# Kernel tuning notes

Measured on AMD Instinct MI355X. Metric: run time of the kernel, lower is better.

The kernel has to match this reference:

```python
import jax, jax.numpy as jnp
import numpy as np
import math
from jax import lax

B, NP1, M, D, H, L, DFF = 16, 65, 256, 512, 8, 3, 2048
EPS_PROJ = 0.01  # MartingaleProjectionLayer is built with epsilon=0.01
LN_EPS = 1e-5


def _pos_encoding(n, d):
    pos = np.arange(n, dtype=np.float32)[:, None]
    div = np.exp(np.arange(0, d, 2, dtype=np.float32) * (-math.log(10000.0) / d))
    pe = np.zeros((n, d), dtype=np.float32)
    pe[:, 0::2] = np.sin(pos * div)
    pe[:, 1::2] = np.cos(pos * div)
    return jnp.asarray(pe)


def setup_inputs() -> dict:
    key = jax.random.key(0)
    ks = jax.random.split(key, 32)
    s = 0.02
    marg = jax.random.uniform(ks[0], (B, NP1, M), jnp.float32)
    marg = marg / marg.sum(axis=-1, keepdims=True)  # proper distributions
    return {
        "marginals": marg,
        "x_grid": jnp.linspace(-3.0, 3.0, M, dtype=jnp.float32),
        "conv_w": jax.random.normal(ks[1], (128, 1, 5), jnp.float32) * s,
        "conv_b": jax.random.normal(ks[2], (128,), jnp.float32) * s,
        "fc_w": jax.random.normal(ks[3], (128, D), jnp.float32) * s,
        "fc_b": jax.random.normal(ks[4], (D,), jnp.float32) * s,
        "ln0_g": jnp.ones((D,), jnp.float32),
        "ln0_b": jnp.zeros((D,), jnp.float32),
        "pos_enc": _pos_encoding(NP1, D),
        "qkv_w": jax.random.normal(ks[5], (L, 3 * D, D), jnp.float32) * s,
        "qkv_b": jax.random.normal(ks[6], (L, 3 * D), jnp.float32) * s,
        "out_w": jax.random.normal(ks[7], (L, D, D), jnp.float32) * s,
        "out_b": jax.random.normal(ks[8], (L, D), jnp.float32) * s,
        "ln1_g": jnp.ones((L, D), jnp.float32),
        "ln1_b": jnp.zeros((L, D), jnp.float32),
        "ff1_w": jax.random.normal(ks[9], (L, DFF, D), jnp.float32) * s,
        "ff1_b": jax.random.normal(ks[10], (L, DFF), jnp.float32) * s,
        "ff2_w": jax.random.normal(ks[11], (L, D, DFF), jnp.float32) * s,
        "ff2_b": jax.random.normal(ks[12], (L, D), jnp.float32) * s,
        "ln2_g": jnp.ones((L, D), jnp.float32),
        "ln2_b": jnp.zeros((L, D), jnp.float32),
        "u_w": jax.random.normal(ks[13], (M, D), jnp.float32) * s,
        "u_b": jax.random.normal(ks[14], (M,), jnp.float32) * s,
        "h_w": jax.random.normal(ks[15], (M, D), jnp.float32) * s,
        "h_b": jax.random.normal(ks[16], (M,), jnp.float32) * s,
    }


def _ln(x, g, b):
    mu = x.mean(axis=-1, keepdims=True)
    var = ((x - mu) ** 2).mean(axis=-1, keepdims=True)
    return (x - mu) * lax.rsqrt(var + LN_EPS) * g + b


def _gelu(x):
    return jax.nn.gelu(x, approximate=False)  # torch default exact GELU


def reference(marginals, x_grid, conv_w, conv_b, fc_w, fc_b, ln0_g, ln0_b,
              pos_enc, qkv_w, qkv_b, out_w, out_b, ln1_g, ln1_b,
              ff1_w, ff1_b, ff2_w, ff2_b, ln2_g, ln2_b, u_w, u_b, h_w, h_b):
    b, np1, m = marginals.shape
    n = np1 - 1
    d = fc_w.shape[1]
    nh = H
    dh = d // nh

    # ---- marginal embedding: Conv1d(1,128,k=5,pad=2) -> mean over grid -> FC+LN+GELU
    x = marginals.reshape(b * np1, 1, m)
    y = lax.conv_general_dilated(x, conv_w, (1,), [(2, 2)],
                                 dimension_numbers=("NCH", "OIH", "NCH"))
    y = y + conv_b[None, :, None]          # (b*np1, 128, m)
    emb = y.mean(axis=2)                   # (b*np1, 128)
    emb = _gelu(_ln(emb @ fc_w + fc_b, ln0_g, ln0_b))
    xs = emb.reshape(b, np1, d) + pos_enc[None, :np1, :]

    # ---- post-norm transformer encoder (dropout off / eval mode)
    scale = 1.0 / math.sqrt(dh)
    for l in range(L):
        qkv = xs @ qkv_w[l].T + qkv_b[l]                        # (b, s, 3d)
        q, k, v = jnp.split(qkv, 3, axis=-1)
        q = q.reshape(b, np1, nh, dh).transpose(0, 2, 1, 3)
        k = k.reshape(b, np1, nh, dh).transpose(0, 2, 1, 3)
        v = v.reshape(b, np1, nh, dh).transpose(0, 2, 1, 3)
        att = jax.nn.softmax(jnp.einsum("bhqd,bhkd->bhqk", q, k) * scale, axis=-1)
        o = jnp.einsum("bhqk,bhkd->bhqd", att, v)
        o = o.transpose(0, 2, 1, 3).reshape(b, np1, d)
        o = o @ out_w[l].T + out_b[l]
        xs = _ln(xs + o, ln1_g[l], ln1_b[l])
        ff = _gelu(xs @ ff1_w[l].T + ff1_b[l]) @ ff2_w[l].T + ff2_b[l]
        xs = _ln(xs + ff, ln2_g[l], ln2_b[l])

    u_pot = xs @ u_w.T + u_b                                    # (b, np1, M)
    h_raw = xs[:, :n, :] @ h_w.T + h_b                          # (b, n, M)

    # ---- vectorized martingale projection over all N timesteps
    x_diff = x_grid[:, None] - x_grid[None, :]                  # (M, M)
    h_kernel = h_raw[..., None] * x_diff                        # (b, n, M, M)
    P = jax.nn.softmax(h_kernel / EPS_PROJ, axis=-1)
    expected_next = jnp.einsum("bnij,j->bni", P, x_grid)
    drift = expected_next - x_grid                              # (b, n, M)
    mu = marginals[:, :n, :]
    weight_drift = (mu * drift).sum(axis=-1, keepdims=True)
    correction = weight_drift / (mu.sum(axis=-1, keepdims=True) + 1e-8)
    h_pot = h_raw - correction
    return (u_pot, h_pot)
```

## Files before the change

### kernel.cpp

```cpp
#include <hip/hip_runtime.h>
#include <math.h>


#define BT   1040
#define NP1  65
#define Dm   512
#define MG   256

typedef short short8 __attribute__((ext_vector_type(8)));
typedef float f32x4  __attribute__((ext_vector_type(4)));
typedef unsigned short u16;

__device__ __forceinline__ size_t pidx(int r, int c, int KB) {
  return ((size_t)((r >> 6) * KB + (c >> 6)) * 8 + ((c & 63) >> 3)) * 512
       + (size_t)((r & 63) * 8 + (c & 7));
}

__device__ __forceinline__ u16 f2bf(float f) {
  unsigned int u = __float_as_uint(f);
  u += 0x7FFF + ((u >> 16) & 1);
  return (u16)(u >> 16);
}

__device__ __forceinline__ float gelu_exact(float x) {
  return 0.5f * x * (1.0f + erff(x * 0.70710678118654752f));
}

__device__ __forceinline__ void async16(const u16* g, u16* l) {
  __builtin_amdgcn_global_load_lds(
      (const __attribute__((address_space(1))) unsigned int*)g,
      (__attribute__((address_space(3))) unsigned int*)l, 16, 0, 0);
}

__device__ __forceinline__ float wred(float v) {
#pragma unroll
  for (int o = 32; o; o >>= 1) v += __shfl_xor(v, o, 64);
  return v;
}

__device__ __forceinline__ float block_reduce_sum(float v, float* s) {
#pragma unroll
  for (int off = 32; off; off >>= 1) v += __shfl_down(v, off, 64);
  int lane = threadIdx.x & 63, wid = threadIdx.x >> 6;
  __syncthreads();
  if (lane == 0) s[wid] = v;
  __syncthreads();
  return s[0] + s[1] + s[2] + s[3];
}

__device__ __forceinline__ float f_closed(float a) {
  const float tf = 2.3529411765f;
  float t = a * tf;
  float s = fabsf(t);
  float E;
  if (s < 1e-4f) {
    E = 127.5f - 5461.25f * t;
  } else {
    float u = s * 256.0f;
    float term2 = (u < 80.0f) ? 256.0f / expm1f(u) : 0.0f;
    float Epos = 1.0f / expm1f(s) - term2;
    E = (t > 0.0f) ? Epos : 255.0f - Epos;
  }
  return -3.0f + 0.0235294118f * E;
}

__global__ __launch_bounds__(256) void prep_kernel(
    const float* __restrict__ qkv_w, const float* __restrict__ out_w,
    const float* __restrict__ ff1_w, const float* __restrict__ ff2_w,
    const float* __restrict__ u_w,   const float* __restrict__ h_w,
    u16* __restrict__ wdst,
    const float* __restrict__ marg, const float* __restrict__ conv_w,
    const float* __restrict__ conv_b, const float* __restrict__ fc_w,
    const float* __restrict__ fc_b, const float* __restrict__ g,
    const float* __restrict__ bb, const float* __restrict__ pos,
    float* __restrict__ xs, u16* __restrict__ xsb)
{
  const int tid = threadIdx.x;
  if (blockIdx.x < 512) {
    const size_t O1 = 2359296, O2 = 3145728, O3 = 6291456;
    const size_t O4 = 9437184, O5 = 9568256, TOT4 = 9699328 / 4;
    for (size_t e4 = (size_t)blockIdx.x * 256 + tid; e4 < TOT4;
         e4 += (size_t)512 * 256) {
      size_t e = e4 * 4;
      const float* src; size_t base; int n, k, KB;
      if (e < O1)      { size_t r = e;      src = qkv_w + r; base = 0;
                         n = (int)(r >> 9);  k = (int)(r & 511);  KB = 8; }
      else if (e < O2) { size_t r = e - O1; src = out_w + r; base = O1;
                         n = (int)(r >> 9);  k = (int)(r & 511);  KB = 8; }
      else if (e < O3) { size_t r = e - O2; src = ff1_w + r; base = O2;
                         n = (int)(r >> 9);  k = (int)(r & 511);  KB = 8; }
      else if (e < O4) { size_t r = e - O3; src = ff2_w + r; base = O3;
                         n = (int)(r >> 11); k = (int)(r & 2047); KB = 32; }
      else if (e < O5) { size_t r = e - O4; src = u_w + r;   base = O4;
                         n = (int)(r >> 9);  k = (int)(r & 511);  KB = 8; }
      else             { size_t r = e - O5; src = h_w + r;   base = O4;
                         n = 256 + (int)(r >> 9); k = (int)(r & 511); KB = 8; }
      float4 v = *(const float4*)src;
      unsigned int lo = (unsigned int)f2bf(v.x) | ((unsigned int)f2bf(v.y) << 16);
      unsigned int hi = (unsigned int)f2bf(v.z) | ((unsigned int)f2bf(v.w) << 16);
      *(uint2*)(wdst + base + pidx(n, k, KB)) = make_uint2(lo, hi);
    }
    return;
  }
  __shared__ float es[4][128];
  __shared__ float sS[4];
  __shared__ float edge[4][4];
  __shared__ float red[4];
  const int t0 = (blockIdx.x - 512) * 4;
  const int lane = tid & 63, wave = tid >> 6;
  {
    float4 mv = *(const float4*)(marg + (size_t)(t0 + wave) * MG + lane * 4);
    float S = wred(mv.x + mv.y + mv.z + mv.w);
    if (lane == 0) sS[wave] = S;
  }
  if (tid < 16) {
    int k = tid >> 2, e = tid & 3;
    int idx = (e < 2) ? e : (e + 252);
    edge[k][e] = marg[(size_t)(t0 + k) * MG + idx];
  }
  __syncthreads();
  if (tid < 128) {
    int o = tid;
    float w0 = conv_w[o*5+0], w1 = conv_w[o*5+1], w2 = conv_w[o*5+2];
    float w3 = conv_w[o*5+3], w4 = conv_w[o*5+4], cb = conv_b[o];
#pragma unroll
    for (int k = 0; k < 4; ++k) {
      float S = sS[k];
      float x0 = edge[k][0], x1 = edge[k][1], x254 = edge[k][2], x255 = edge[k][3];
      es[k][o] = (w0*(S - x254 - x255) + w1*(S - x255) + w2*S
                + w3*(S - x0) + w4*(S - x0 - x1)) * (1.0f/256.0f) + cb;
    }
  }
  __syncthreads();
  float b0 = fc_b[tid], b1 = fc_b[tid + 256];
  float z[4][2];
#pragma unroll
  for (int k = 0; k < 4; ++k) { z[k][0] = b0; z[k][1] = b1; }
#pragma unroll 4
  for (int o = 0; o < 128; ++o) {
    float f0 = fc_w[(size_t)o*Dm + tid];
    float f1 = fc_w[(size_t)o*Dm + tid + 256];
#pragma unroll
    for (int k = 0; k < 4; ++k) {
      float e = es[k][o];
      z[k][0] += e * f0; z[k][1] += e * f1;
    }
  }
  float g0 = g[tid], g1 = g[tid+256], e0 = bb[tid], e1 = bb[tid+256];
#pragma unroll
  for (int k = 0; k < 4; ++k) {
    float mu = block_reduce_sum(z[k][0] + z[k][1], red) * (1.0f/512.0f);
    float d0 = z[k][0] - mu, d1 = z[k][1] - mu;
    float var = block_reduce_sum(d0*d0 + d1*d1, red) * (1.0f/512.0f);
    float inv = rsqrtf(var + 1e-5f);
    int t = t0 + k, p = t % NP1;
    float y0 = gelu_exact(d0*inv*g0 + e0) + pos[(size_t)p*Dm + tid];
    float y1 = gelu_exact(d1*inv*g1 + e1) + pos[(size_t)p*Dm + tid + 256];
    xs[(size_t)t*Dm + tid]        = y0;
    xs[(size_t)t*Dm + tid + 256]  = y1;
    xsb[pidx(t, tid, 8)]          = f2bf(y0);
    xsb[pidx(t, tid + 256, 8)]    = f2bf(y1);
  }
}

template<int MODE>
__global__ __launch_bounds__(256) void gemm_mfma(
    const u16* __restrict__ A, const u16* __restrict__ Bw,
    const float* __restrict__ bias, float* __restrict__ Cf,
    u16* __restrict__ Cb, int Mrows, int N, int K)
{
  __shared__ u16 Asl[2][4096];
  __shared__ u16 Bsl[2][4096];
  const int tid = threadIdx.x;
  const int row0 = blockIdx.y * 64, col0 = blockIdx.x * 64;
  const int lane = tid & 63, wave = tid >> 6;
  const int wm = (wave >> 1) * 32, wn = (wave & 1) * 32;
  const int l15 = lane & 15, q = lane >> 4;
  const int KB = K >> 6;

  f32x4 acc[2][2];
  acc[0][0] = (f32x4){0,0,0,0}; acc[0][1] = (f32x4){0,0,0,0};
  acc[1][0] = (f32x4){0,0,0,0}; acc[1][1] = (f32x4){0,0,0,0};

  const size_t abase = (size_t)blockIdx.y * KB * 4096 + (size_t)lane * 8;
  const size_t bbase = (size_t)blockIdx.x * KB * 4096 + (size_t)lane * 8;
  const int c0w = wave * 2;

#pragma unroll
  for (int i = 0; i < 2; ++i) {
    int c = c0w + i;
    async16(A + abase + (size_t)c * 512, &Asl[0][(size_t)(c * 64 + lane) * 8]);
    async16(Bw + bbase + (size_t)c * 512, &Bsl[0][(size_t)(c * 64 + lane) * 8]);
  }

  const int nk = K >> 6;
  for (int t = 0; t < nk; ++t) {
    const int cur = t & 1;
    if (t + 1 < nk) {
      const int nxt = cur ^ 1;
#pragma unroll
      for (int i = 0; i < 2; ++i) {
        int c = c0w + i;
        async16(A + abase + (size_t)((t + 1) * 8 + c) * 512,
                &Asl[nxt][(size_t)(c * 64 + lane) * 8]);
        async16(Bw + bbase + (size_t)((t + 1) * 8 + c) * 512,
                &Bsl[nxt][(size_t)(c * 64 + lane) * 8]);
      }
      asm volatile("s_waitcnt vmcnt(4)" ::: "memory");
    } else {
      asm volatile("s_waitcnt vmcnt(0)" ::: "memory");
    }
    __builtin_amdgcn_s_barrier();
#pragma unroll
    for (int tt = 0; tt < 2; ++tt) {
      int cc = tt * 4 + q;
      short8 af[2], bf[2];
#pragma unroll
      for (int mi = 0; mi < 2; ++mi)
        af[mi] = *(short8*)&Asl[cur][(size_t)(cc*64 + wm + mi*16 + l15) * 8];
#pragma unroll
      for (int ni = 0; ni < 2; ++ni)
        bf[ni] = *(short8*)&Bsl[cur][(size_t)(cc*64 + wn + ni*16 + l15) * 8];
#pragma unroll
      for (int mi = 0; mi < 2; ++mi)
#pragma unroll
        for (int ni = 0; ni < 2; ++ni)
          acc[mi][ni] = __builtin_amdgcn_mfma_f32_16x16x32_bf16(
              af[mi], bf[ni], acc[mi][ni], 0, 0, 0);
    }
    __builtin_amdgcn_s_barrier();
  }

#pragma unroll
  for (int mi = 0; mi < 2; ++mi) {
#pragma unroll
    for (int ni = 0; ni < 2; ++ni) {
      int col = col0 + wn + ni*16 + l15;
#pragma unroll
      for (int r = 0; r < 4; ++r) {
        int row = row0 + wm + mi*16 + q*4 + r;
        if (row < Mrows) {
          float v = acc[mi][ni][r];
          if (MODE == 0) {
            Cf[(size_t)row*N + col] = v + bias[col];
          } else {
            Cb[pidx(row, col, 32)] = f2bf(gelu_exact(v + bias[col]));
          }
        }
      }
    }
  }
}

template<int KK, int EPI>
__global__ __launch_bounds__(256) void fused_row(
    const u16* __restrict__ A, const u16* __restrict__ Bw,
    const float* __restrict__ bias,
    float* __restrict__ xs, u16* __restrict__ xsb,
    const float* __restrict__ g, const float* __restrict__ bb,
    const float* __restrict__ bias2,
    const float* __restrict__ marg, const float* __restrict__ xg,
    float* __restrict__ outu, float* __restrict__ outh)
{
  constexpr int KB  = KK >> 6;
  constexpr int KC  = (KK < 1024) ? KK : 1024;
  constexpr int NCH = KK / KC;
  __shared__ u16 Alds[16 * KC];
  __shared__ float red[4][16];
  __shared__ float red2[4][16];
  const int tid = threadIdx.x, lane = tid & 63, wave = tid >> 6;
  const int l15 = lane & 15, q = lane >> 4;
  const int r0 = blockIdx.x * 16;
  const int rb = r0 >> 6, ro = r0 & 63;
  const int gc0 = wave * 128;

  f32x4 acc[8];
#pragma unroll
  for (int i = 0; i < 8; ++i) acc[i] = (f32x4){0,0,0,0};

  for (int ch = 0; ch < NCH; ++ch) {
    const int kc = ch * KC;
    __syncthreads();
    for (int idx = tid; idx < 2 * KC; idx += 256) {
      int rloc = idx & 15, cg = idx >> 4;
      int kbg = (kc >> 6) + (cg >> 3), cc = cg & 7;
      async16(A + ((size_t)(rb * KB + kbg) * 8 + cc) * 512 + (ro + rloc) * 8,
              &Alds[(size_t)idx * 8]);
    }
    asm volatile("s_waitcnt vmcnt(0)" ::: "memory");
    __syncthreads();

    constexpr int S = KC / 32;
    short8 bcur[8], bnxt[8];
    {
      int kk = kc + q * 8;
      int kbg = kk >> 6, cc = (kk & 63) >> 3;
#pragma unroll
      for (int i = 0; i < 8; ++i) {
        int nb = (gc0 >> 6) + (i >> 2), nn = (i & 3) * 16 + l15;
        bcur[i] = *(const short8*)&Bw[((size_t)(nb * KB + kbg) * 8 + cc) * 512
                                      + nn * 8];
      }
    }
    for (int s = 0; s < S; ++s) {
      if (s + 1 < S) {
        int kk = kc + (s + 1) * 32 + q * 8;
        int kbg = kk >> 6, cc = (kk & 63) >> 3;
#pragma unroll
        for (int i = 0; i < 8; ++i) {
          int nb = (gc0 >> 6) + (i >> 2), nn = (i & 3) * 16 + l15;
          bnxt[i] = *(const short8*)&Bw[((size_t)(nb * KB + kbg) * 8 + cc) * 512
                                        + nn * 8];
        }
      }
      short8 af = *(const short8*)&Alds[(size_t)((s * 4 + q) * 16 + l15) * 8];
#pragma unroll
      for (int i = 0; i < 8; ++i)
        acc[i] = __builtin_amdgcn_mfma_f32_16x16x32_bf16(af, bcur[i], acc[i], 0, 0, 0);
#pragma unroll
      for (int i = 0; i < 8; ++i) bcur[i] = bnxt[i];
    }
  }

  if (EPI == 0) {
    float vv[8][4];
#pragma unroll
    for (int i = 0; i < 8; ++i) {
      int col = gc0 + i*16 + l15;
      float bcol = bias[col];
#pragma unroll
      for (int r = 0; r < 4; ++r) {
        int gr = r0 + q*4 + r;
        vv[i][r] = acc[i][r] + bcol + xs[(size_t)gr * Dm + col];
      }
    }
    float ps[4];
#pragma unroll
    for (int r = 0; r < 4; ++r) {
      float s = 0.f;
#pragma unroll
      for (int i = 0; i < 8; ++i) s += vv[i][r];
      ps[r] = s;
    }
#pragma unroll
    for (int o = 1; o < 16; o <<= 1)
#pragma unroll
      for (int r = 0; r < 4; ++r) ps[r] += __shfl_xor(ps[r], o, 64);
    if (l15 == 0)
#pragma unroll
      for (int r = 0; r < 4; ++r) red[wave][q*4 + r] = ps[r];
    __syncthreads();
    float mu[4];
#pragma unroll
    for (int r = 0; r < 4; ++r) {
      int rr = q*4 + r;
      mu[r] = (red[0][rr] + red[1][rr] + red[2][rr] + red[3][rr]) * (1.0f/512.0f);
    }
    float ps2[4];
#pragma unroll
    for (int r = 0; r < 4; ++r) {
      float s = 0.f;
#pragma unroll
      for (int i = 0; i < 8; ++i) { float d = vv[i][r] - mu[r]; s += d * d; }
      ps2[r] = s;
    }
#pragma unroll
    for (int o = 1; o < 16; o <<= 1)
#pragma unroll
      for (int r = 0; r < 4; ++r) ps2[r] += __shfl_xor(ps2[r], o, 64);
    if (l15 == 0)
#pragma unroll
      for (int r = 0; r < 4; ++r) red2[wave][q*4 + r] = ps2[r];
    __syncthreads();
    float inv[4];
#pragma unroll
    for (int r = 0; r < 4; ++r) {
      int rr = q*4 + r;
      inv[r] = rsqrtf((red2[0][rr] + red2[1][rr] + red2[2][rr] + red2[3][rr])
                      * (1.0f/512.0f) + 1e-5f);
    }
#pragma unroll
    for (int i = 0; i < 8; ++i) {
      int col = gc0 + i*16 + l15;
      float gc = g[col], bc = bb[col];
#pragma unroll
      for (int r = 0; r < 4; ++r) {
        int gr = r0 + q*4 + r;
        float y = (vv[i][r] - mu[r]) * inv[r] * gc + bc;
        xs[(size_t)gr * Dm + col] = y;
        xsb[pidx(gr, col, 8)] = f2bf(y);
      }
    }
  } else {
    float va[8][4];
    if (wave >= 2) {
      float wd[4] = {0.f,0.f,0.f,0.f}, ms[4] = {0.f,0.f,0.f,0.f};
#pragma unroll
      for (int i = 0; i < 8; ++i) {
        int hcol = (gc0 - 256) + i*16 + l15;
        float bcol = bias2[hcol];
        float xv = xg[hcol];
#pragma unroll
        for (int r = 0; r < 4; ++r) {
          int gr = r0 + q*4 + r;
          float a = acc[i][r] + bcol;
          va[i][r] = a;
          float uvm = marg[(size_t)gr * MG + hcol];
          wd[r] += uvm * (f_closed(a) - xv);
          ms[r] += uvm;
        }
      }
#pragma unroll
      for (int o = 1; o < 16; o <<= 1)
#pragma unroll
        for (int r = 0; r < 4; ++r) {
          wd[r] += __shfl_xor(wd[r], o, 64);
          ms[r] += __shfl_xor(ms[r], o, 64);
        }
      if (l15 == 0)
#pragma unroll
        for (int r = 0; r < 4; ++r) {
          red[wave][q*4 + r]  = wd[r];
          red2[wave][q*4 + r] = ms[r];
        }
    }
    __syncthreads();
    if (wave < 2) {
#pragma unroll
      for (int i = 0; i < 8; ++i) {
        int col = gc0 + i*16 + l15;
        float bcol = bias[col];
#pragma unroll
        for (int r = 0; r < 4; ++r) {
          int gr = r0 + q*4 + r;
          outu[(size_t)gr * MG + col] = acc[i][r] + bcol;
        }
      }
    } else {
#pragma unroll
      for (int i = 0; i < 8; ++i) {
        int hcol = (gc0 - 256) + i*16 + l15;
#pragma unroll
        for (int r = 0; r < 4; ++r) {
          int rr = q*4 + r;
          int gr = r0 + rr;
          int b = gr / NP1, n = gr - b * NP1;
          if (n < 64) {
            float corr = (red[2][rr] + red[3][rr])
                       / (red2[2][rr] + red2[3][rr] + 1e-8f);
            outh[(size_t)(b * 64 + n) * MG + hcol] = va[i][r] - corr;
          }
        }
      }
    }
  }
}

__global__ __launch_bounds__(256) void attn_kernel(
    const float* __restrict__ qkv, u16* __restrict__ obufb)
{
  __shared__ float qv[65][67];
  __shared__ float ks[65][67];
  __shared__ float ss[65][67];
  const int b = blockIdx.x >> 3, h = blockIdx.x & 7;
  const int tid = threadIdx.x;
  const float* base = qkv + (size_t)b * NP1 * 1536 + h * 64;
  for (int idx = tid; idx < NP1 * 16; idx += 256) {
    int t = idx >> 4, c = (idx & 15) << 2;
    const float* p = base + (size_t)t * 1536 + c;
    float4 q4 = *(const float4*)(p);
    float4 k4 = *(const float4*)(p + 512);
    qv[t][c] = q4.x; qv[t][c+1] = q4.y; qv[t][c+2] = q4.z; qv[t][c+3] = q4.w;
    ks[t][c] = k4.x; ks[t][c+1] = k4.y; ks[t][c+2] = k4.z; ks[t][c+3] = k4.w;
  }
  __syncthreads();
#pragma unroll
  for (int it = 0; it < 2; ++it) {
    int tile = it * 256 + tid;
    if (tile < 289) {
      int ti = (tile / 17) * 4, tj = (tile % 17) * 4;
      const float* qr[4]; const float* kr[4];
#pragma unroll
      for (int i = 0; i < 4; ++i) { qr[i] = qv[min(ti + i, 64)]; kr[i] = ks[min(tj + i, 64)]; }
      float acc[4][4] = {};
      for (int d = 0; d < 64; ++d) {
        float a[4], bvv[4];
#pragma unroll
        for (int i = 0; i < 4; ++i) { a[i] = qr[i][d]; bvv[i] = kr[i][d]; }
#pragma unroll
        for (int i = 0; i < 4; ++i)
#pragma unroll
          for (int j = 0; j < 4; ++j) acc[i][j] += a[i] * bvv[j];
      }
#pragma unroll
      for (int i = 0; i < 4; ++i)
        if (ti + i < 65)
#pragma unroll
          for (int j = 0; j < 4; ++j)
            if (tj + j < 65) ss[ti + i][tj + j] = acc[i][j] * 0.125f;
    }
  }
  __syncthreads();
  for (int idx = tid; idx < NP1 * 16; idx += 256) {
    int t = idx >> 4, c = (idx & 15) << 2;
    float4 v4 = *(const float4*)(base + (size_t)t * 1536 + 1024 + c);
    qv[t][c] = v4.x; qv[t][c+1] = v4.y; qv[t][c+2] = v4.z; qv[t][c+3] = v4.w;
  }
  if (tid < 65) {
    float mx = -1e30f;
    for (int j = 0; j < 65; ++j) mx = fmaxf(mx, ss[tid][j]);
    float s = 0.0f;
    for (int j = 0; j < 65; ++j) { float e = expf(ss[tid][j] - mx); ss[tid][j] = e; s += e; }
    float inv = 1.0f / s;
    for (int j = 0; j < 65; ++j) ss[tid][j] *= inv;
  }
  __syncthreads();
#pragma unroll
  for (int it = 0; it < 2; ++it) {
    int tile = it * 256 + tid;
    if (tile < 272) {
      int ti = (tile >> 4) * 4, d0 = (tile & 15) * 4;
      const float* sr[4];
#pragma unroll
      for (int i = 0; i < 4; ++i) sr[i] = ss[min(ti + i, 64)];
      float acc[4][4] = {};
      for (int j = 0; j < 65; ++j) {
        float v0 = qv[j][d0], v1 = qv[j][d0+1], v2 = qv[j][d0+2], v3 = qv[j][d0+3];
#pragma unroll
        for (int i = 0; i < 4; ++i) {
          float s = sr[i][j];
          acc[i][0] += s * v0; acc[i][1] += s * v1;
          acc[i][2] += s * v2; acc[i][3] += s * v3;
        }
      }
#pragma unroll
      for (int i = 0; i < 4; ++i)
        if (ti + i < 65) {
          ushort4 o;
          o.x = f2bf(acc[i][0]); o.y = f2bf(acc[i][1]);
          o.z = f2bf(acc[i][2]); o.w = f2bf(acc[i][3]);
          *(ushort4*)(obufb + pidx(b * NP1 + ti + i, h * 64 + d0, 8)) = o;
        }
    }
  }
}

extern "C" void kernel_launch(void* const* d_in, const int* in_sizes, int n_in,
                              void* d_out, int out_size, void* d_ws, size_t ws_size,
                              hipStream_t stream)
{
  const float* marg   = (const float*)d_in[0];
  const float* xg     = (const float*)d_in[1];
  const float* conv_w = (const float*)d_in[2];
  const float* conv_b = (const float*)d_in[3];
  const float* fc_w   = (const float*)d_in[4];
  const float* fc_b   = (const float*)d_in[5];
  const float* ln0_g  = (const float*)d_in[6];
  const float* ln0_b  = (const float*)d_in[7];
  const float* pos    = (const float*)d_in[8];
  const float* qkv_w  = (const float*)d_in[9];
  const float* qkv_b  = (const float*)d_in[10];
  const float* out_w  = (const float*)d_in[11];
  const float* out_b  = (const float*)d_in[12];
  const float* ln1_g  = (const float*)d_in[13];
  const float* ln1_b  = (const float*)d_in[14];
  const float* ff1_w  = (const float*)d_in[15];
  const float* ff1_b  = (const float*)d_in[16];
  const float* ff2_w  = (const float*)d_in[17];
  const float* ff2_b  = (const float*)d_in[18];
  const float* ln2_g  = (const float*)d_in[19];
  const float* ln2_b  = (const float*)d_in[20];
  const float* u_w    = (const float*)d_in[21];
  const float* u_b    = (const float*)d_in[22];
  const float* h_w    = (const float*)d_in[23];
  const float* h_b    = (const float*)d_in[24];
  float* out = (float*)d_out;

  float* ws = (float*)d_ws;
  float* xs      = ws;
  float* qkvbuf  = ws + 532480;
  u16*   xsb     = (u16*)(ws + 2129920);
  u16*   obufb   = (u16*)(ws + 2408448);
  u16*   ffb     = (u16*)(ws + 2686976);
  u16*   wbf     = (u16*)(ws + 3801088);

  const u16* qkv_bw = wbf;
  const u16* out_bw = wbf + 2359296;
  const u16* ff1_bw = wbf + 3145728;
  const u16* ff2_bw = wbf + 6291456;
  const u16* uh_bw  = wbf + 9437184;

  prep_kernel<<<772, 256, 0, stream>>>(
      qkv_w, out_w, ff1_w, ff2_w, u_w, h_w, wbf,
      marg, conv_w, conv_b, fc_w, fc_b, ln0_g, ln0_b, pos, xs, xsb);

  for (int l = 0; l < 3; ++l) {
    gemm_mfma<0><<<dim3(24, 17), 256, 0, stream>>>(
        xsb, qkv_bw + (size_t)l*786432, qkv_b + l*1536, qkvbuf,
        nullptr, BT, 1536, 512);
    attn_kernel<<<128, 256, 0, stream>>>(qkvbuf, obufb);
    fused_row<512, 0><<<65, 256, 0, stream>>>(
        obufb, out_bw + (size_t)l*262144, out_b + l*512,
        xs, xsb, ln1_g + l*512, ln1_b + l*512,
        nullptr, nullptr, nullptr, nullptr, nullptr);
    gemm_mfma<1><<<dim3(32, 17), 256, 0, stream>>>(
        xsb, ff1_bw + (size_t)l*1048576, ff1_b + l*2048, nullptr,
        ffb, BT, 2048, 512);
    fused_row<2048, 0><<<65, 256, 0, stream>>>(
        ffb, ff2_bw + (size_t)l*1048576, ff2_b + l*512,
        xs, xsb, ln2_g + l*512, ln2_b + l*512,
        nullptr, nullptr, nullptr, nullptr, nullptr);
  }

  fused_row<512, 1><<<65, 256, 0, stream>>>(
      xsb, uh_bw, u_b,
      nullptr, nullptr, nullptr, nullptr,
      h_b, marg, xg, out, out + 1040*256);
}
```

Baseline: 420.6 us.

## Fuse QKV projection into attention kernel and widen fused_row to 512 threads

```diff
diff --git a/kernel.cpp b/kernel.cpp
--- a/kernel.cpp
+++ b/kernel.cpp
@@ -20,6 +20,10 @@
   unsigned int u = __float_as_uint(f);
   u += 0x7FFF + ((u >> 16) & 1);
   return (u16)(u >> 16);
+}
+
+__device__ __forceinline__ float bf2f(u16 v) {
+  return __uint_as_float((unsigned int)v << 16);
 }
 
 __device__ __forceinline__ float gelu_exact(float x) {
@@ -169,8 +173,8 @@
     const float* __restrict__ bias, float* __restrict__ Cf,
     u16* __restrict__ Cb, int Mrows, int N, int K)
 {
-  __shared__ u16 Asl[2][4096];
-  __shared__ u16 Bsl[2][4096];
+  __shared__ alignas(16) u16 Asl[2][4096];
+  __shared__ alignas(16) u16 Bsl[2][4096];
   const int tid = threadIdx.x;
   const int row0 = blockIdx.y * 64, col0 = blockIdx.x * 64;
   const int lane = tid & 63, wave = tid >> 6;
@@ -252,8 +256,168 @@
   }
 }
 
+__global__ __launch_bounds__(256) void fused_qkv_attn(
+    const u16* __restrict__ xsb, const u16* __restrict__ qkvw,
+    const float* __restrict__ qkvb, u16* __restrict__ obufb)
+{
+  __shared__ alignas(16) u16 stbuf[10240];
+  __shared__ alignas(16) float qf[65][67];
+  __shared__ alignas(16) float kf[65][67];
+  __shared__ alignas(16) u16   vb[65][68];
+  u16* sta = stbuf;
+  float (*ss)[67] = (float (*)[67])stbuf;
+
+  const int b = blockIdx.x >> 3, h = blockIdx.x & 7;
+  const int tid = threadIdx.x, lane = tid & 63, wave = tid >> 6;
+  const int l15 = lane & 15, q = lane >> 4;
+  const int rowg0 = b * NP1;
+
+  f32x4 acc[5][3];
+#pragma unroll
+  for (int rt = 0; rt < 5; ++rt)
+#pragma unroll
+    for (int j = 0; j < 3; ++j) acc[rt][j] = (f32x4){0,0,0,0};
+
+  for (int ch = 0; ch < 4; ++ch) {
+    __syncthreads();
+    for (int idx = tid; idx < 16 * 80; idx += 256) {
+      int kg = idx / 80, rl = idx - kg * 80;
+      int r = rowg0 + min(rl, 64);
+      async16(xsb + pidx(r, ch * 128 + kg * 8, 8), &sta[(size_t)idx * 8]);
+    }
+    asm volatile("s_waitcnt vmcnt(0)" ::: "memory");
+    __syncthreads();
+
+    short8 bcur[3], bnxt[3];
+#pragma unroll
+    for (int j = 0; j < 3; ++j) {
+      int f = wave * 3 + j, region = f >> 2, sub = f & 3;
+      int nb = region * 8 + h, nn = sub * 16 + l15;
+      int kk = ch * 128 + q * 8;
+      int kbg = kk >> 6, cc = (kk & 63) >> 3;
+      bcur[j] = *(const short8*)&qkvw[((size_t)(nb * 8 + kbg) * 8 + cc) * 512
+                                      + nn * 8];
+    }
+#pragma unroll
+    for (int s = 0; s < 4; ++s) {
+      if (s + 1 < 4) {
+#pragma unroll
+        for (int j = 0; j < 3; ++j) {
+          int f = wave * 3 + j, region = f >> 2, sub = f & 3;
+          int nb = region * 8 + h, nn = sub * 16 + l15;
+          int kk = ch * 128 + (s + 1) * 32 + q * 8;
+          int kbg = kk >> 6, cc = (kk & 63) >> 3;
+          bnxt[j] = *(const short8*)&qkvw[((size_t)(nb * 8 + kbg) * 8 + cc) * 512
+                                          + nn * 8];
+        }
+      }
+      short8 af[5];
+#pragma unroll
+      for (int rt = 0; rt < 5; ++rt)
+        af[rt] = *(short8*)&sta[(size_t)((s * 4 + q) * 80 + rt * 16 + l15) * 8];
+#pragma unroll
+      for (int rt = 0; rt < 5; ++rt)
+#pragma unroll
+        for (int j = 0; j < 3; ++j)
+          acc[rt][j] = __builtin_amdgcn_mfma_f32_16x16x32_bf16(
+              af[rt], bcur[j], acc[rt][j], 0, 0, 0);
+#pragma unroll
+      for (int j = 0; j < 3; ++j) bcur[j] = bnxt[j];
+    }
+  }
+
+#pragma unroll
+  for (int rt = 0; rt < 5; ++rt) {
+#pragma unroll
+    for (int j = 0; j < 3; ++j) {
+      int f = wave * 3 + j, region = f >> 2, sub = f & 3;
+      int cw = sub * 16 + l15;
+      float bias = qkvb[region * 512 + h * 64 + cw];
+#pragma unroll
+      for (int r = 0; r < 4; ++r) {
+        int row = rt * 16 + q * 4 + r;
+        if (row < 65) {
+          float v = acc[rt][j][r] + bias;
+          if      (region == 0) qf[row][cw] = v;
+          else if (region == 1) kf[row][cw] = v;
+          else                  vb[row][cw] = f2bf(v);
+        }
+      }
+    }
+  }
+  __syncthreads();
+
+#pragma unroll
+  for (int it = 0; it < 2; ++it) {
+    int tile = it * 256 + tid;
+    if (tile < 289) {
+      int ti = (tile / 17) * 4, tj = (tile % 17) * 4;
+      const float* qr[4]; const float* kr[4];
+#pragma unroll
+      for (int i = 0; i < 4; ++i) { qr[i] = qf[min(ti + i, 64)]; kr[i] = kf[min(tj + i, 64)]; }
+      float a4[4][4] = {};
+      for (int d = 0; d < 64; ++d) {
+        float a[4], bvv[4];
+#pragma unroll
+        for (int i = 0; i < 4; ++i) { a[i] = qr[i][d]; bvv[i] = kr[i][d]; }
+#pragma unroll
+        for (int i = 0; i < 4; ++i)
+#pragma unroll
+          for (int j = 0; j < 4; ++j) a4[i][j] += a[i] * bvv[j];
+      }
+#pragma unroll
+      for (int i = 0; i < 4; ++i)
+        if (ti + i < 65)
+#pragma unroll
+          for (int j = 0; j < 4; ++j)
+            if (tj + j < 65) ss[ti + i][tj + j] = a4[i][j] * 0.125f;
+    }
+  }
+  __syncthreads();
+
+  if (tid < 65) {
+    float mx = -1e30f;
+    for (int j = 0; j < 65; ++j) mx = fmaxf(mx, ss[tid][j]);
+    float s = 0.0f;
+    for (int j = 0; j < 65; ++j) { float e = expf(ss[tid][j] - mx); ss[tid][j] = e; s += e; }
+    float inv = 1.0f / s;
+    for (int j = 0; j < 65; ++j) ss[tid][j] *= inv;
+  }
+  __syncthreads();
+
+#pragma unroll
+  for (int it = 0; it < 2; ++it) {
+    int tile = it * 256 + tid;
+    if (tile < 272) {
+      int ti = (tile >> 4) * 4, d0 = (tile & 15) * 4;
+      const float* sr[4];
+#pragma unroll
+      for (int i = 0; i < 4; ++i) sr[i] = ss[min(ti + i, 64)];
+      float a4[4][4] = {};
+      for (int j = 0; j < 65; ++j) {
+        float v0 = bf2f(vb[j][d0]),   v1 = bf2f(vb[j][d0+1]);
+        float v2 = bf2f(vb[j][d0+2]), v3 = bf2f(vb[j][d0+3]);
+#pragma unroll
+        for (int i = 0; i < 4; ++i) {
+          float s = sr[i][j];
+          a4[i][0] += s * v0; a4[i][1] += s * v1;
+          a4[i][2] += s * v2; a4[i][3] += s * v3;
+        }
+      }
+#pragma unroll
+      for (int i = 0; i < 4; ++i)
+        if (ti + i < 65) {
+          ushort4 o;
+          o.x = f2bf(a4[i][0]); o.y = f2bf(a4[i][1]);
+          o.z = f2bf(a4[i][2]); o.w = f2bf(a4[i][3]);
+          *(ushort4*)(obufb + pidx(b * NP1 + ti + i, h * 64 + d0, 8)) = o;
+        }
+    }
+  }
+}
+
 template<int KK, int EPI>
-__global__ __launch_bounds__(256) void fused_row(
+__global__ __launch_bounds__(512) void fused_row(
     const u16* __restrict__ A, const u16* __restrict__ Bw,
     const float* __restrict__ bias,
     float* __restrict__ xs, u16* __restrict__ xsb,
@@ -265,23 +429,24 @@
   constexpr int KB  = KK >> 6;
   constexpr int KC  = (KK < 1024) ? KK : 1024;
   constexpr int NCH = KK / KC;
-  __shared__ u16 Alds[16 * KC];
-  __shared__ float red[4][16];
-  __shared__ float red2[4][16];
+  __shared__ alignas(16) u16 Alds[16 * KC];
+  __shared__ float red[8][16];
+  __shared__ float red2[8][16];
   const int tid = threadIdx.x, lane = tid & 63, wave = tid >> 6;
   const int l15 = lane & 15, q = lane >> 4;
   const int r0 = blockIdx.x * 16;
   const int rb = r0 >> 6, ro = r0 & 63;
-  const int gc0 = wave * 128;
-
-  f32x4 acc[8];
-#pragma unroll
-  for (int i = 0; i < 8; ++i) acc[i] = (f32x4){0,0,0,0};
+  const int gc0 = wave * 64;
+  const int nb = wave;
+
+  f32x4 acc[4];
+#pragma unroll
+  for (int i = 0; i < 4; ++i) acc[i] = (f32x4){0,0,0,0};
 
   for (int ch = 0; ch < NCH; ++ch) {
     const int kc = ch * KC;
     __syncthreads();
-    for (int idx = tid; idx < 2 * KC; idx += 256) {
+    for (int idx = tid; idx < 2 * KC; idx += 512) {
       int rloc = idx & 15, cg = idx >> 4;
       int kbg = (kc >> 6) + (cg >> 3), cc = cg & 7;
       async16(A + ((size_t)(rb * KB + kbg) * 8 + cc) * 512 + (ro + rloc) * 8,
@@ -291,41 +456,37 @@
     __syncthreads();
 
     constexpr int S = KC / 32;
-    short8 bcur[8], bnxt[8];
+    short8 bcur[4], bnxt[4];
     {
       int kk = kc + q * 8;
       int kbg = kk >> 6, cc = (kk & 63) >> 3;
 #pragma unroll
-      for (int i = 0; i < 8; ++i) {
-        int nb = (gc0 >> 6) + (i >> 2), nn = (i & 3) * 16 + l15;
+      for (int i = 0; i < 4; ++i)
         bcur[i] = *(const short8*)&Bw[((size_t)(nb * KB + kbg) * 8 + cc) * 512
-                                      + nn * 8];
-      }
+                                      + (i * 16 + l15) * 8];
     }
     for (int s = 0; s < S; ++s) {
       if (s + 1 < S) {
         int kk = kc + (s + 1) * 32 + q * 8;
         int kbg = kk >> 6, cc = (kk & 63) >> 3;
 #pragma unroll
-        for (int i = 0; i < 8; ++i) {
-          int nb = (gc0 >> 6) + (i >> 2), nn = (i & 3) * 16 + l15;
+        for (int i = 0; i < 4; ++i)
           bnxt[i] = *(const short8*)&Bw[((size_t)(nb * KB + kbg) * 8 + cc) * 512
-                                        + nn * 8];
-        }
+                                        + (i * 16 + l15) * 8];
       }
       short8 af = *(const short8*)&Alds[(size_t)((s * 4 + q) * 16 + l15) * 8];
 #pragma unroll
-      for (int i = 0; i < 8; ++i)
+      for (int i = 0; i < 4; ++i)
         acc[i] = __builtin_amdgcn_mfma_f32_16x16x32_bf16(af, bcur[i], acc[i], 0, 0, 0);
 #pragma unroll
-      for (int i = 0; i < 8; ++i) bcur[i] = bnxt[i];
+      for (int i = 0; i < 4; ++i) bcur[i] = bnxt[i];
     }
   }
 
   if (EPI == 0) {
-    float vv[8][4];
-#pragma unroll
-    for (int i = 0; i < 8; ++i) {
+    float vv[4][4];
+#pragma unroll
+    for (int i = 0; i < 4; ++i) {
       int col = gc0 + i*16 + l15;
       float bcol = bias[col];
 #pragma unroll
@@ -339,7 +500,7 @@
     for (int r = 0; r < 4; ++r) {
       float s = 0.f;
 #pragma unroll
-      for (int i = 0; i < 8; ++i) s += vv[i][r];
+      for (int i = 0; i < 4; ++i) s += vv[i][r];
       ps[r] = s;
     }
 #pragma unroll
@@ -354,14 +515,17 @@
 #pragma unroll
     for (int r = 0; r < 4; ++r) {
       int rr = q*4 + r;
-      mu[r] = (red[0][rr] + red[1][rr] + red[2][rr] + red[3][rr]) * (1.0f/512.0f);
+      float s = 0.f;
+#pragma unroll
+      for (int w = 0; w < 8; ++w) s += red[w][rr];
+      mu[r] = s * (1.0f/512.0f);
     }
     float ps2[4];
 #pragma unroll
     for (int r = 0; r < 4; ++r) {
       float s = 0.f;
 #pragma unroll
-      for (int i = 0; i < 8; ++i) { float d = vv[i][r] - mu[r]; s += d * d; }
+      for (int i = 0; i < 4; ++i) { float d = vv[i][r] - mu[r]; s += d * d; }
       ps2[r] = s;
     }
 #pragma unroll
@@ -376,11 +540,13 @@
 #pragma unroll
     for (int r = 0; r < 4; ++r) {
       int rr = q*4 + r;
-      inv[r] = rsqrtf((red2[0][rr] + red2[1][rr] + red2[2][rr] + red2[3][rr])
-                      * (1.0f/512.0f) + 1e-5f);
-    }
-#pragma unroll
-    for (int i = 0; i < 8; ++i) {
+      float s = 0.f;
+#pragma unroll
+      for (int w = 0; w < 8; ++w) s += red2[w][rr];
+      inv[r] = rsqrtf(s * (1.0f/512.0f) + 1e-5f);
+    }
+#pragma unroll
+    for (int i = 0; i < 4; ++i) {
       int col = gc0 + i*16 + l15;
       float gc = g[col], bc = bb[col];
 #pragma unroll
@@ -392,11 +558,11 @@
       }
     }
   } else {
-    float va[8][4];
-    if (wave >= 2) {
+    float va[4][4];
+    if (wave >= 4) {
       float wd[4] = {0.f,0.f,0.f,0.f}, ms[4] = {0.f,0.f,0.f,0.f};
 #pragma unroll
-      for (int i = 0; i < 8; ++i) {
+      for (int i = 0; i < 4; ++i) {
         int hcol = (gc0 - 256) + i*16 + l15;
         float bcol = bias2[hcol];
         float xv = xg[hcol];
@@ -425,9 +591,9 @@
         }
     }
     __syncthreads();
-    if (wave < 2) {
-#pragma unroll
-      for (int i = 0; i < 8; ++i) {
+    if (wave < 4) {
+#pragma unroll
+      for (int i = 0; i < 4; ++i) {
         int col = gc0 + i*16 + l15;
         float bcol = bias[col];
 #pragma unroll
@@ -438,109 +604,21 @@
       }
     } else {
 #pragma unroll
-      for (int i = 0; i < 8; ++i) {
+      for (int i = 0; i < 4; ++i) {
         int hcol = (gc0 - 256) + i*16 + l15;
 #pragma unroll
         for (int r = 0; r < 4; ++r) {
           int rr = q*4 + r;
           int gr = r0 + rr;
-          int b = gr / NP1, n = gr - b * NP1;
+          int bI = gr / NP1, n = gr - bI * NP1;
           if (n < 64) {
-            float corr = (red[2][rr] + red[3][rr])
-                       / (red2[2][rr] + red2[3][rr] + 1e-8f);
-            outh[(size_t)(b * 64 + n) * MG + hcol] = va[i][r] - corr;
+            float num = red[4][rr] + red[5][rr] + red[6][rr] + red[7][rr];
+            float den = red2[4][rr] + red2[5][rr] + red2[6][rr] + red2[7][rr];
+            float corr = num / (den + 1e-8f);
+            outh[(size_t)(bI * 64 + n) * MG + hcol] = va[i][r] - corr;
           }
         }
       }
-    }
-  }
-}
-
-__global__ __launch_bounds__(256) void attn_kernel(
-    const float* __restrict__ qkv, u16* __restrict__ obufb)
-{
-  __shared__ float qv[65][67];
-  __shared__ float ks[65][67];
-  __shared__ float ss[65][67];
-  const int b = blockIdx.x >> 3, h = blockIdx.x & 7;
-  const int tid = threadIdx.x;
-  const float* base = qkv + (size_t)b * NP1 * 1536 + h * 64;
-  for (int idx = tid; idx < NP1 * 16; idx += 256) {
-    int t = idx >> 4, c = (idx & 15) << 2;
-    const float* p = base + (size_t)t * 1536 + c;
-    float4 q4 = *(const float4*)(p);
-    float4 k4 = *(const float4*)(p + 512);
-    qv[t][c] = q4.x; qv[t][c+1] = q4.y; qv[t][c+2] = q4.z; qv[t][c+3] = q4.w;
-    ks[t][c] = k4.x; ks[t][c+1] = k4.y; ks[t][c+2] = k4.z; ks[t][c+3] = k4.w;
-  }
-  __syncthreads();
-#pragma unroll
-  for (int it = 0; it < 2; ++it) {
-    int tile = it * 256 + tid;
-    if (tile < 289) {
-      int ti = (tile / 17) * 4, tj = (tile % 17) * 4;
-      const float* qr[4]; const float* kr[4];
-#pragma unroll
-      for (int i = 0; i < 4; ++i) { qr[i] = qv[min(ti + i, 64)]; kr[i] = ks[min(tj + i, 64)]; }
-      float acc[4][4] = {};
-      for (int d = 0; d < 64; ++d) {
-        float a[4], bvv[4];
-#pragma unroll
-        for (int i = 0; i < 4; ++i) { a[i] = qr[i][d]; bvv[i] = kr[i][d]; }
-#pragma unroll
-        for (int i = 0; i < 4; ++i)
-#pragma unroll
-          for (int j = 0; j < 4; ++j) acc[i][j] += a[i] * bvv[j];
-      }
-#pragma unroll
-      for (int i = 0; i < 4; ++i)
-        if (ti + i < 65)
-#pragma unroll
-          for (int j = 0; j < 4; ++j)
-            if (tj + j < 65) ss[ti + i][tj + j] = acc[i][j] * 0.125f;
-    }
-  }
-  __syncthreads();
-  for (int idx = tid; idx < NP1 * 16; idx += 256) {
-    int t = idx >> 4, c = (idx & 15) << 2;
-    float4 v4 = *(const float4*)(base + (size_t)t * 1536 + 1024 + c);
-    qv[t][c] = v4.x; qv[t][c+1] = v4.y; qv[t][c+2] = v4.z; qv[t][c+3] = v4.w;
-  }
-  if (tid < 65) {
-    float mx = -1e30f;
-    for (int j = 0; j < 65; ++j) mx = fmaxf(mx, ss[tid][j]);
-    float s = 0.0f;
-    for (int j = 0; j < 65; ++j) { float e = expf(ss[tid][j] - mx); ss[tid][j] = e; s += e; }
-    float inv = 1.0f / s;
-    for (int j = 0; j < 65; ++j) ss[tid][j] *= inv;
-  }
-  __syncthreads();
-#pragma unroll
-  for (int it = 0; it < 2; ++it) {
-    int tile = it * 256 + tid;
-    if (tile < 272) {
-      int ti = (tile >> 4) * 4, d0 = (tile & 15) * 4;
-      const float* sr[4];
-#pragma unroll
-      for (int i = 0; i < 4; ++i) sr[i] = ss[min(ti + i, 64)];
-      float acc[4][4] = {};
-      for (int j = 0; j < 65; ++j) {
-        float v0 = qv[j][d0], v1 = qv[j][d0+1], v2 = qv[j][d0+2], v3 = qv[j][d0+3];
-#pragma unroll
-        for (int i = 0; i < 4; ++i) {
-          float s = sr[i][j];
-          acc[i][0] += s * v0; acc[i][1] += s * v1;
-          acc[i][2] += s * v2; acc[i][3] += s * v3;
-        }
-      }
-#pragma unroll
-      for (int i = 0; i < 4; ++i)
-        if (ti + i < 65) {
-          ushort4 o;
-          o.x = f2bf(acc[i][0]); o.y = f2bf(acc[i][1]);
-          o.z = f2bf(acc[i][2]); o.w = f2bf(acc[i][3]);
-          *(ushort4*)(obufb + pidx(b * NP1 + ti + i, h * 64 + d0, 8)) = o;
-        }
     }
   }
 }
@@ -578,7 +656,6 @@
 
   float* ws = (float*)d_ws;
   float* xs      = ws;
-  float* qkvbuf  = ws + 532480;
   u16*   xsb     = (u16*)(ws + 2129920);
   u16*   obufb   = (u16*)(ws + 2408448);
   u16*   ffb     = (u16*)(ws + 2686976);
@@ -595,24 +672,22 @@
       marg, conv_w, conv_b, fc_w, fc_b, ln0_g, ln0_b, pos, xs, xsb);
 
   for (int l = 0; l < 3; ++l) {
-    gemm_mfma<0><<<dim3(24, 17), 256, 0, stream>>>(
-        xsb, qkv_bw + (size_t)l*786432, qkv_b + l*1536, qkvbuf,
-        nullptr, BT, 1536, 512);
-    attn_kernel<<<128, 256, 0, stream>>>(qkvbuf, obufb);
-    fused_row<512, 0><<<65, 256, 0, stream>>>(
+    fused_qkv_attn<<<128, 256, 0, stream>>>(
+        xsb, qkv_bw + (size_t)l*786432, qkv_b + l*1536, obufb);
+    fused_row<512, 0><<<65, 512, 0, stream>>>(
         obufb, out_bw + (size_t)l*262144, out_b + l*512,
         xs, xsb, ln1_g + l*512, ln1_b + l*512,
         nullptr, nullptr, nullptr, nullptr, nullptr);
     gemm_mfma<1><<<dim3(32, 17), 256, 0, stream>>>(
         xsb, ff1_bw + (size_t)l*1048576, ff1_b + l*2048, nullptr,
         ffb, BT, 2048, 512);
-    fused_row<2048, 0><<<65, 256, 0, stream>>>(
+    fused_row<2048, 0><<<65, 512, 0, stream>>>(
         ffb, ff2_bw + (size_t)l*1048576, ff2_b + l*512,
         xs, xsb, ln2_g + l*512, ln2_b + l*512,
         nullptr, nullptr, nullptr, nullptr, nullptr);
   }
 
-  fused_row<512, 1><<<65, 256, 0, stream>>>(
+  fused_row<512, 1><<<65, 512, 0, stream>>>(
       xsb, uh_bw, u_b,
       nullptr, nullptr, nullptr, nullptr,
       h_b, marg, xg, out, out + 1040*256);
```

New measurement: 379.1 us (median of 2 runs). -9.9%, faster.
